# Kernel optimization log

Hardware: AMD Instinct MI355X
Metric: run time of the kernel (lower is better)

Reference implementation:

```python
import jax, jax.numpy as jnp
import numpy as np

N_VOX = 4_000_000
N_CLUSTS = 50_000


def setup_inputs() -> dict:
    key = jax.random.key(0)
    k1, k2 = jax.random.split(key)
    data = jax.random.normal(k1, (N_VOX, 6), dtype=jnp.float32)
    clust_ids = jax.random.randint(k2, (N_VOX,), 0, N_CLUSTS, dtype=jnp.int32)
    return {"data": data, "clust_ids": clust_ids, "n_clusts": N_CLUSTS}


def reference(data, clust_ids, n_clusts):
    # COORD_COLS = (1, 2, 3): columns [batch, x, y, z, value, shape]
    coords = data[:, 1:4].astype(jnp.float32)            # [N, 3]
    cid = clust_ids
    ones = jnp.ones((coords.shape[0],), coords.dtype)
    size = jax.ops.segment_sum(ones, cid, num_segments=n_clusts)          # [K]
    csum = jax.ops.segment_sum(coords, cid, num_segments=n_clusts)        # [K, 3]
    center = csum / jnp.maximum(size, 1.0)[:, None]                        # [K, 3]

    x = coords - center[cid]                                               # [N, 3]
    # Per-cluster scatter matrix A = x^T x (batched over clusters)
    A = jax.ops.segment_sum(x[:, :, None] * x[:, None, :], cid,
                            num_segments=n_clusts)                         # [K, 3, 3]

    w, v = jnp.linalg.eigh(A)            # ascending eigenvalues, like torch
    w2 = w[:, 2]
    safe_w2 = jnp.where(w2 > 0, w2, 1.0)
    dirwt = 1.0 - w[:, 1] / safe_w2      # [K]
    B = A / safe_w2[:, None, None]       # [K, 3, 3]
    v0 = v[:, :, 2]                      # principal axis, [K, 3]

    # Orient principal axis: sc = sum_i x0_i * ||x_i - x0_i v0||
    x0 = jnp.einsum('nd,nd->n', x, v0[cid])                                # [N]
    xp0 = x - x0[:, None] * v0[cid]                                        # [N, 3]
    np0 = jnp.linalg.norm(xp0, axis=1)                                     # [N]
    sc = jax.ops.segment_sum(x0 * np0, cid, num_segments=n_clusts)         # [K]
    v0 = jnp.where(sc[:, None] < 0, -v0, v0) * dirwt[:, None]

    # Singleton clusters (size < 2): center + 12 zeros + size
    multi = size >= 2.0
    B = jnp.where(multi[:, None, None], B, 0.0)
    v0 = jnp.where(multi[:, None], v0, 0.0)

    feats = jnp.concatenate(
        [center, B.reshape(-1, 9), v0, size[:, None]], axis=1)            # [K, 16]
    return feats
```

## Files before the change

kernel.cpp:

```cpp
#include <hip/hip_runtime.h>
#include <math.h>


#define NB_CL   64
#define CAP2    6144
#define NB_MAX  1024

__device__ inline void eig3_sym(double a00, double a01, double a02,
                                double a11, double a12, double a22,
                                double& w0, double& w1, double& w2,
                                double v[3]) {
    double p1 = a01 * a01 + a02 * a02 + a12 * a12;
    double q  = (a00 + a11 + a22) / 3.0;
    double d0 = a00 - q, d1 = a11 - q, d2 = a22 - q;
    double p2 = d0 * d0 + d1 * d1 + d2 * d2 + 2.0 * p1;
    double p  = sqrt(p2 / 6.0);
    if (p < 1e-300) {
        w0 = w1 = w2 = q;
        v[0] = 0.0; v[1] = 0.0; v[2] = 1.0;
        return;
    }
    double ip = 1.0 / p;
    double b00 = d0 * ip, b11 = d1 * ip, b22 = d2 * ip;
    double b01 = a01 * ip, b02 = a02 * ip, b12 = a12 * ip;
    double detB = b00 * (b11 * b22 - b12 * b12)
                - b01 * (b01 * b22 - b12 * b02)
                + b02 * (b01 * b12 - b11 * b02);
    double r = detB * 0.5;
    r = fmin(1.0, fmax(-1.0, r));
    double phi = acos(r) / 3.0;
    w2 = q + 2.0 * p * cos(phi);
    w0 = q + 2.0 * p * cos(phi + 2.0943951023931953);
    w1 = 3.0 * q - w2 - w0;

    double r0x = a00 - w2, r0y = a01,       r0z = a02;
    double r1x = a01,      r1y = a11 - w2,  r1z = a12;
    double r2x = a02,      r2y = a12,       r2z = a22 - w2;

    double c0x = r0y * r1z - r0z * r1y;
    double c0y = r0z * r1x - r0x * r1z;
    double c0z = r0x * r1y - r0y * r1x;
    double n0  = c0x * c0x + c0y * c0y + c0z * c0z;

    double c1x = r0y * r2z - r0z * r2y;
    double c1y = r0z * r2x - r0x * r2z;
    double c1z = r0x * r2y - r0y * r2x;
    double n1  = c1x * c1x + c1y * c1y + c1z * c1z;

    double c2x = r1y * r2z - r1z * r2y;
    double c2y = r1z * r2x - r1x * r2z;
    double c2z = r1x * r2y - r1y * r2x;
    double n2  = c2x * c2x + c2y * c2y + c2z * c2z;

    double vx, vy, vz, nn;
    if (n0 >= n1 && n0 >= n2) { vx = c0x; vy = c0y; vz = c0z; nn = n0; }
    else if (n1 >= n2)        { vx = c1x; vy = c1y; vz = c1z; nn = n1; }
    else                      { vx = c2x; vy = c2y; vz = c2z; nn = n2; }
    if (nn < 1e-300) {
        v[0] = 0.0; v[1] = 0.0; v[2] = 1.0;
        return;
    }
    double inv = rsqrt(nn);
    v[0] = vx * inv; v[1] = vy * inv; v[2] = vz * inv;
}

#define P1_BLOCK 1024
#define P1_ITEMS 8

__global__ void p1_bucket(const float* __restrict__ data,
                          const int* __restrict__ cid,
                          unsigned int* __restrict__ gcnt,
                          float4* __restrict__ bbuf,
                          int n_vox, int nbuckets) {
    __shared__ unsigned int hist[NB_MAX];
    __shared__ unsigned int base[NB_MAX];
    const int tid = threadIdx.x;
    const int per_round = P1_BLOCK * P1_ITEMS;
    const int total_rounds = (n_vox + per_round - 1) / per_round;

    for (int r = blockIdx.x; r < total_rounds; r += gridDim.x) {
        const int start = r * per_round;
        for (int j = tid; j < nbuckets; j += P1_BLOCK) hist[j] = 0;
        __syncthreads();

        int   bk[P1_ITEMS];
        int   cd[P1_ITEMS];
        float px[P1_ITEMS], py[P1_ITEMS], pz[P1_ITEMS];
        unsigned int rk[P1_ITEMS];
#pragma unroll
        for (int k = 0; k < P1_ITEMS; ++k) {
            int i = start + tid + k * P1_BLOCK;
            if (i < n_vox) {
                int c = cid[i];
                cd[k] = c & (NB_CL - 1);
                bk[k] = c >> 6;
                const float* row = data + (size_t)i * 6;
                px[k] = row[1]; py[k] = row[2]; pz[k] = row[3];
                rk[k] = atomicAdd(&hist[bk[k]], 1u);
            } else {
                bk[k] = -1;
            }
        }
        __syncthreads();
        for (int j = tid; j < nbuckets; j += P1_BLOCK) {
            unsigned int h = hist[j];
            base[j] = h ? atomicAdd(&gcnt[j], h) : 0u;
        }
        __syncthreads();
#pragma unroll
        for (int k = 0; k < P1_ITEMS; ++k) {
            if (bk[k] >= 0) {
                unsigned int pos = base[bk[k]] + rk[k];
                if (pos < (unsigned int)CAP2) {
                    bbuf[(size_t)bk[k] * CAP2 + pos] =
                        make_float4(px[k], py[k], pz[k], __int_as_float(cd[k]));
                }
            }
        }
        __syncthreads();
    }
}

__global__ __launch_bounds__(512) void p2_features(
        const unsigned int* __restrict__ gcnt,
        const float4* __restrict__ bbuf,
        float* __restrict__ out, int C) {
    __shared__ float sx[CAP2];
    __shared__ float sy[CAP2];
    __shared__ float sz[CAP2];
    __shared__ unsigned int hist[NB_CL];
    __shared__ unsigned int basex[NB_CL];
    __shared__ unsigned int hist2[NB_CL];

    const int b   = blockIdx.x;
    const int tid = threadIdx.x;
    const int bcnt = min((int)gcnt[b], CAP2);
    const float4* src = bbuf + (size_t)b * CAP2;
    const float*  srcw = (const float*)src;

    if (tid < NB_CL) { hist[tid] = 0; hist2[tid] = 0; }
    __syncthreads();

    for (int base_i = 0; base_i < bcnt; base_i += 2048) {
        int i0 = base_i + tid, i1 = i0 + 512, i2 = i0 + 1024, i3 = i0 + 1536;
        int c0 = -1, c1 = -1, c2 = -1, c3 = -1;
        if (i0 < bcnt) c0 = __float_as_int(srcw[4 * i0 + 3]) & (NB_CL - 1);
        if (i1 < bcnt) c1 = __float_as_int(srcw[4 * i1 + 3]) & (NB_CL - 1);
        if (i2 < bcnt) c2 = __float_as_int(srcw[4 * i2 + 3]) & (NB_CL - 1);
        if (i3 < bcnt) c3 = __float_as_int(srcw[4 * i3 + 3]) & (NB_CL - 1);
        if (c0 >= 0) atomicAdd(&hist[c0], 1u);
        if (c1 >= 0) atomicAdd(&hist[c1], 1u);
        if (c2 >= 0) atomicAdd(&hist[c2], 1u);
        if (c3 >= 0) atomicAdd(&hist[c3], 1u);
    }
    __syncthreads();

    if (tid < NB_CL) {
        unsigned int h = hist[tid];
        unsigned int inc = h;
#pragma unroll
        for (int off = 1; off < NB_CL; off <<= 1) {
            unsigned int t = __shfl_up(inc, off);
            if (tid >= off) inc += t;
        }
        basex[tid] = inc - h;
    }
    __syncthreads();

    for (int base_i = 0; base_i < bcnt; base_i += 2048) {
        int i0 = base_i + tid, i1 = i0 + 512, i2 = i0 + 1024, i3 = i0 + 1536;
        bool v0 = i0 < bcnt, v1 = i1 < bcnt, v2 = i2 < bcnt, v3 = i3 < bcnt;
        float4 p0, p1, p2, p3;
        if (v0) p0 = src[i0];
        if (v1) p1 = src[i1];
        if (v2) p2 = src[i2];
        if (v3) p3 = src[i3];
        if (v0) { int c = __float_as_int(p0.w) & (NB_CL - 1); unsigned r = atomicAdd(&hist2[c], 1u); unsigned q = basex[c] + r; sx[q] = p0.x; sy[q] = p0.y; sz[q] = p0.z; }
        if (v1) { int c = __float_as_int(p1.w) & (NB_CL - 1); unsigned r = atomicAdd(&hist2[c], 1u); unsigned q = basex[c] + r; sx[q] = p1.x; sy[q] = p1.y; sz[q] = p1.z; }
        if (v2) { int c = __float_as_int(p2.w) & (NB_CL - 1); unsigned r = atomicAdd(&hist2[c], 1u); unsigned q = basex[c] + r; sx[q] = p2.x; sy[q] = p2.y; sz[q] = p2.z; }
        if (v3) { int c = __float_as_int(p3.w) & (NB_CL - 1); unsigned r = atomicAdd(&hist2[c], 1u); unsigned q = basex[c] + r; sx[q] = p3.x; sy[q] = p3.y; sz[q] = p3.z; }
    }
    __syncthreads();

    const int w    = tid >> 6;
    const int lane = tid & 63;

    float k0 = 0.f, k1 = 0.f, k2 = 0.f, k3 = 0.f, k4 = 0.f;
    float k5 = 0.f, k6 = 0.f, k7 = 0.f, k8 = 0.f;

#pragma unroll
    for (int jj = 0; jj < 8; ++jj) {
        const int lc = (w << 3) | jj;
        const int n  = (int)hist[lc];
        const unsigned int nb = basex[lc];
        float s0 = 0.f, s1 = 0.f, s2 = 0.f, s3 = 0.f, s4 = 0.f;
        float s5 = 0.f, s6 = 0.f, s7 = 0.f, s8 = 0.f;
        for (int j = lane; j < n; j += 64) {
            float x = sx[nb + j], y = sy[nb + j], z = sz[nb + j];
            s0 += x;     s1 += y;     s2 += z;
            s3 += x * x; s4 += x * y; s5 += x * z;
            s6 += y * y; s7 += y * z; s8 += z * z;
        }
#pragma unroll
        for (int d = 32; d > 0; d >>= 1) {
            s0 += __shfl_xor(s0, d); s1 += __shfl_xor(s1, d); s2 += __shfl_xor(s2, d);
            s3 += __shfl_xor(s3, d); s4 += __shfl_xor(s4, d); s5 += __shfl_xor(s5, d);
            s6 += __shfl_xor(s6, d); s7 += __shfl_xor(s7, d); s8 += __shfl_xor(s8, d);
        }
        if (lane == jj) {
            k0 = s0; k1 = s1; k2 = s2; k3 = s3; k4 = s4;
            k5 = s5; k6 = s6; k7 = s7; k8 = s8;
        }
    }

    float cenx = 0.f, ceny = 0.f, cenz = 0.f;
    float evx = 0.f, evy = 0.f, evz = 0.f, fdw = 0.f;
    if (lane < 8) {
        const int lc = (w << 3) | lane;
        const int cl = b * NB_CL + lc;
        const int n  = (int)hist[lc];
        double dn = (double)n;
        double nd = (double)max(n, 1);
        double cx = (double)k0 / nd;
        double cy = (double)k1 / nd;
        double cz = (double)k2 / nd;

        double axx = (double)k3 - dn * cx * cx;
        double axy = (double)k4 - dn * cx * cy;
        double axz = (double)k5 - dn * cx * cz;
        double ayy = (double)k6 - dn * cy * cy;
        double ayz = (double)k7 - dn * cy * cz;
        double azz = (double)k8 - dn * cz * cz;

        double w0, w1, w2, v[3];
        eig3_sym(axx, axy, axz, ayy, ayz, azz, w0, w1, w2, v);

        double safe_w2 = (w2 > 0.0) ? w2 : 1.0;
        double isw = 1.0 / safe_w2;
        bool multi = (n >= 2);

        cenx = (float)cx; ceny = (float)cy; cenz = (float)cz;
        evx = (float)v[0]; evy = (float)v[1]; evz = (float)v[2];
        fdw = (float)(1.0 - w1 / safe_w2);

        if (cl < C) {
            float b3  = multi ? (float)(axx * isw) : 0.0f;
            float b4  = multi ? (float)(axy * isw) : 0.0f;
            float b5  = multi ? (float)(axz * isw) : 0.0f;
            float b7  = multi ? (float)(ayy * isw) : 0.0f;
            float b8  = multi ? (float)(ayz * isw) : 0.0f;
            float b11 = multi ? (float)(azz * isw) : 0.0f;
            float4* o = (float4*)(out + (size_t)cl * 16);
            o[0] = make_float4(cenx, ceny, cenz, b3);
            o[1] = make_float4(b4, b5, b4, b7);
            o[2] = make_float4(b8, b5, b8, b11);
        }
    }

#pragma unroll 1
    for (int jj = 0; jj < 8; ++jj) {
        const int lc = (w << 3) | jj;
        const int cl = b * NB_CL + lc;
        if (cl >= C) continue;
        const int n = (int)hist[lc];
        const unsigned int nb = basex[lc];
        const float fcx = __shfl(cenx, jj), fcy = __shfl(ceny, jj), fcz = __shfl(cenz, jj);
        const float vx = __shfl(evx, jj), vy = __shfl(evy, jj), vz = __shfl(evz, jj);
        const float dwv = __shfl(fdw, jj);
        float sc = 0.0f;
        for (int j = lane; j < n; j += 64) {
            float x = sx[nb + j] - fcx, y = sy[nb + j] - fcy, z = sz[nb + j] - fcz;
            float x0 = x * vx + y * vy + z * vz;
            float qx = x - x0 * vx, qy = y - x0 * vy, qz = z - x0 * vz;
            sc += x0 * sqrtf(qx * qx + qy * qy + qz * qz);
        }
#pragma unroll
        for (int d = 32; d > 0; d >>= 1) sc += __shfl_xor(sc, d);

        if (lane == 0) {
            float sgn = (sc < 0.0f) ? -1.0f : 1.0f;
            float m = (n >= 2) ? sgn * dwv : 0.0f;
            ((float4*)(out + (size_t)cl * 16))[3] =
                make_float4(vx * m, vy * m, vz * m, (float)n);
        }
    }
}

#define FXP_SCALE 131072.0f
#define FXP_BIAS  4194304
#define FXP_INV   (1.0 / 131072.0)

__device__ __forceinline__ unsigned int fxp_enc(float v) {
    return (unsigned int)(__float2int_rn(v * FXP_SCALE) + FXP_BIAS);
}
__device__ __forceinline__ double fxp_dec(unsigned int s, int n) {
    return (double)((long long)s - (long long)n * FXP_BIAS) * FXP_INV;
}

__global__ void k1_accum(const float* __restrict__ data,
                         const int* __restrict__ cid,
                         unsigned long long* __restrict__ acc,
                         int n_vox) {
    int stride = gridDim.x * blockDim.x;
    for (int i = blockIdx.x * blockDim.x + threadIdx.x; i < n_vox; i += stride) {
        int c = cid[i];
        const float* row = data + (size_t)i * 6;
        float x = row[1], y = row[2], z = row[3];
        unsigned long long* a = acc + (size_t)c * 5;
        unsigned long long p0 = ((unsigned long long)fxp_enc(y)     << 32) | fxp_enc(x);
        unsigned long long p1 = ((unsigned long long)fxp_enc(x * x) << 32) | fxp_enc(z);
        unsigned long long p2 = ((unsigned long long)fxp_enc(x * z) << 32) | fxp_enc(x * y);
        unsigned long long p3 = ((unsigned long long)fxp_enc(y * z) << 32) | fxp_enc(y * y);
        unsigned long long p4 = (1ULL << 32)                               | fxp_enc(z * z);
        atomicAdd(&a[0], p0);
        atomicAdd(&a[1], p1);
        atomicAdd(&a[2], p2);
        atomicAdd(&a[3], p3);
        atomicAdd(&a[4], p4);
    }
}

__global__ void k2_cluster(const unsigned long long* __restrict__ acc,
                           float* __restrict__ wf,
                           float* __restrict__ out, int C) {
    int c = blockIdx.x * blockDim.x + threadIdx.x;
    if (c >= C) return;
    const unsigned long long* a = acc + (size_t)c * 5;
    unsigned long long s0 = a[0], s1 = a[1], s2 = a[2], s3 = a[3], s4 = a[4];
    int n = (int)(s4 >> 32);

    double sx  = fxp_dec((unsigned int)s0,         n);
    double sy  = fxp_dec((unsigned int)(s0 >> 32), n);
    double sz  = fxp_dec((unsigned int)s1,         n);
    double sxx = fxp_dec((unsigned int)(s1 >> 32), n);
    double sxy = fxp_dec((unsigned int)s2,         n);
    double sxz = fxp_dec((unsigned int)(s2 >> 32), n);
    double syy = fxp_dec((unsigned int)s3,         n);
    double syz = fxp_dec((unsigned int)(s3 >> 32), n);
    double szz = fxp_dec((unsigned int)s4,         n);

    double nd = (double)max(n, 1);
    double cx = sx / nd, cy = sy / nd, cz = sz / nd;
    double dn = (double)n;
    double axx = sxx - dn * cx * cx;
    double axy = sxy - dn * cx * cy;
    double axz = sxz - dn * cx * cz;
    double ayy = syy - dn * cy * cy;
    double ayz = syz - dn * cy * cz;
    double azz = szz - dn * cz * cz;

    double w0, w1, w2, v[3];
    eig3_sym(axx, axy, axz, ayy, ayz, azz, w0, w1, w2, v);

    double safe_w2 = (w2 > 0.0) ? w2 : 1.0;
    double dirwt   = 1.0 - w1 / safe_w2;
    double isw     = 1.0 / safe_w2;
    bool multi = (n >= 2);

    float* o = out + (size_t)c * 16;
    o[0] = (float)cx; o[1] = (float)cy; o[2] = (float)cz;
    if (multi) {
        o[3]  = (float)(axx * isw); o[4]  = (float)(axy * isw); o[5]  = (float)(axz * isw);
        o[6]  = (float)(axy * isw); o[7]  = (float)(ayy * isw); o[8]  = (float)(ayz * isw);
        o[9]  = (float)(axz * isw); o[10] = (float)(ayz * isw); o[11] = (float)(azz * isw);
    } else {
        o[3] = 0.f; o[4] = 0.f; o[5] = 0.f; o[6] = 0.f; o[7] = 0.f;
        o[8] = 0.f; o[9] = 0.f; o[10] = 0.f; o[11] = 0.f;
    }
    o[15] = (float)n;

    wf[(size_t)C * 1 + c] = (float)cx;
    wf[(size_t)C * 2 + c] = (float)cy;
    wf[(size_t)C * 3 + c] = (float)cz;
    wf[(size_t)C * 4 + c] = (float)v[0];
    wf[(size_t)C * 5 + c] = (float)v[1];
    wf[(size_t)C * 6 + c] = (float)v[2];
    wf[(size_t)C * 7 + c] = (float)dirwt;
}

__global__ void k3_sc(const float* __restrict__ data,
                      const int* __restrict__ cid,
                      float* __restrict__ wf,
                      int n_vox, int C) {
    const float* cenx = wf + (size_t)C * 1;
    const float* ceny = wf + (size_t)C * 2;
    const float* cenz = wf + (size_t)C * 3;
    const float* v0x  = wf + (size_t)C * 4;
    const float* v0y  = wf + (size_t)C * 5;
    const float* v0z  = wf + (size_t)C * 6;
    float* sc = wf;
    int stride = gridDim.x * blockDim.x;
    for (int i = blockIdx.x * blockDim.x + threadIdx.x; i < n_vox; i += stride) {
        int c = cid[i];
        const float* row = data + (size_t)i * 6;
        float x = row[1] - cenx[c];
        float y = row[2] - ceny[c];
        float z = row[3] - cenz[c];
        float vx = v0x[c], vy = v0y[c], vz = v0z[c];
        float x0 = x * vx + y * vy + z * vz;
        float px = x - x0 * vx;
        float py = y - x0 * vy;
        float pz = z - x0 * vz;
        atomicAdd(&sc[c], x0 * sqrtf(px * px + py * py + pz * pz));
    }
}

__global__ void k4_final(const unsigned long long* __restrict__ acc,
                         const float* __restrict__ wf,
                         float* __restrict__ out, int C) {
    int c = blockIdx.x * blockDim.x + threadIdx.x;
    if (c >= C) return;
    int n = (int)(acc[(size_t)c * 5 + 4] >> 32);
    float scv = wf[c];
    float vx  = wf[(size_t)C * 4 + c];
    float vy  = wf[(size_t)C * 5 + c];
    float vz  = wf[(size_t)C * 6 + c];
    float dir = wf[(size_t)C * 7 + c];
    float sgn = (scv < 0.0f) ? -1.0f : 1.0f;
    float m = (n >= 2) ? sgn * dir : 0.0f;
    float* o = out + (size_t)c * 16;
    o[12] = vx * m;
    o[13] = vy * m;
    o[14] = vz * m;
}

extern "C" void kernel_launch(void* const* d_in, const int* in_sizes, int n_in,
                              void* d_out, int out_size, void* d_ws, size_t ws_size,
                              hipStream_t stream) {
    const float* data = (const float*)d_in[0];
    const int*   cid  = (const int*)d_in[1];
    float* out = (float*)d_out;

    int n_vox = in_sizes[1];
    int C     = out_size / 16;

    int nbuckets = (C + NB_CL - 1) / NB_CL;
    long long expected = (C > 0) ? (long long)n_vox * NB_CL / C : 0;
    size_t gcnt_bytes = ((size_t)nbuckets * 4 + 255) & ~(size_t)255;
    size_t bbuf_bytes = (size_t)nbuckets * CAP2 * 16;
    size_t need = gcnt_bytes + bbuf_bytes;

    if (C > 0 && nbuckets <= NB_MAX && expected <= (CAP2 * 7) / 8 && ws_size >= need) {
        unsigned int* gcnt = (unsigned int*)d_ws;
        float4* bbuf = (float4*)((char*)d_ws + gcnt_bytes);
        hipMemsetAsync(d_ws, 0, gcnt_bytes, stream);
        int total_rounds = (n_vox + P1_BLOCK * P1_ITEMS - 1) / (P1_BLOCK * P1_ITEMS);
        int p1_blocks = total_rounds < 1024 ? total_rounds : 1024;
        if (p1_blocks < 1) p1_blocks = 1;
        p1_bucket<<<p1_blocks, P1_BLOCK, 0, stream>>>(data, cid, gcnt, bbuf, n_vox, nbuckets);
        p2_features<<<nbuckets, 512, 0, stream>>>(gcnt, bbuf, out, C);
    } else {
        unsigned long long* acc = (unsigned long long*)d_ws;
        float* wf = (float*)((char*)d_ws + (size_t)C * 40);
        hipMemsetAsync(d_ws, 0, (size_t)C * 44, stream);
        const int vox_blocks = 4096;
        const int cl_blocks  = (C + 255) / 256;
        k1_accum<<<vox_blocks, 256, 0, stream>>>(data, cid, acc, n_vox);
        k2_cluster<<<cl_blocks, 256, 0, stream>>>(acc, wf, out, C);
        k3_sc<<<vox_blocks, 256, 0, stream>>>(data, cid, wf, n_vox, C);
        k4_final<<<cl_blocks, 256, 0, stream>>>(acc, wf, out, C);
    }
}
```

Before: 140.9 us.

## Stage bucketed voxels in shared memory for coalesced scatter writes

```diff
diff --git a/kernel.cpp b/kernel.cpp
--- a/kernel.cpp
+++ b/kernel.cpp
@@ -66,20 +66,24 @@
 
 #define P1_BLOCK 1024
 #define P1_ITEMS 8
-
-__global__ void p1_bucket(const float* __restrict__ data,
-                          const int* __restrict__ cid,
-                          unsigned int* __restrict__ gcnt,
-                          float4* __restrict__ bbuf,
-                          int n_vox, int nbuckets) {
+#define P1_ROUND (P1_BLOCK * P1_ITEMS)
+
+__global__ __launch_bounds__(P1_BLOCK) void p1_bucket(
+        const float* __restrict__ data,
+        const int* __restrict__ cid,
+        unsigned int* __restrict__ gcnt,
+        float4* __restrict__ bbuf,
+        int n_vox, int nbuckets) {
+    __shared__ float4 ss[P1_ROUND];
     __shared__ unsigned int hist[NB_MAX];
-    __shared__ unsigned int base[NB_MAX];
+    __shared__ unsigned int lbase[NB_MAX];
+    __shared__ unsigned int gbase[NB_MAX];
     const int tid = threadIdx.x;
-    const int per_round = P1_BLOCK * P1_ITEMS;
-    const int total_rounds = (n_vox + per_round - 1) / per_round;
+    const int total_rounds = (n_vox + P1_ROUND - 1) / P1_ROUND;
 
     for (int r = blockIdx.x; r < total_rounds; r += gridDim.x) {
-        const int start = r * per_round;
+        const int start = r * P1_ROUND;
+        const int rtotal = min(P1_ROUND, n_vox - start);
         for (int j = tid; j < nbuckets; j += P1_BLOCK) hist[j] = 0;
         __syncthreads();
 
@@ -92,7 +96,7 @@
             int i = start + tid + k * P1_BLOCK;
             if (i < n_vox) {
                 int c = cid[i];
-                cd[k] = c & (NB_CL - 1);
+                cd[k] = c;
                 bk[k] = c >> 6;
                 const float* row = data + (size_t)i * 6;
                 px[k] = row[1]; py[k] = row[2]; pz[k] = row[3];
@@ -102,20 +106,41 @@
             }
         }
         __syncthreads();
+
+        for (int j = tid; j < nbuckets; j += P1_BLOCK) lbase[j] = hist[j];
+        __syncthreads();
+        for (int off = 1; off < nbuckets; off <<= 1) {
+            unsigned int v = 0;
+            for (int j = tid; j < nbuckets; j += P1_BLOCK)
+                v = (j >= off) ? lbase[j - off] : 0u;
+            __syncthreads();
+            for (int j = tid; j < nbuckets; j += P1_BLOCK)
+                if (j >= off) lbase[j] += v;
+            __syncthreads();
+        }
         for (int j = tid; j < nbuckets; j += P1_BLOCK) {
             unsigned int h = hist[j];
-            base[j] = h ? atomicAdd(&gcnt[j], h) : 0u;
-        }
-        __syncthreads();
+            lbase[j] -= h;
+            gbase[j] = h ? atomicAdd(&gcnt[j], h) : 0u;
+        }
+        __syncthreads();
+
 #pragma unroll
         for (int k = 0; k < P1_ITEMS; ++k) {
             if (bk[k] >= 0) {
-                unsigned int pos = base[bk[k]] + rk[k];
-                if (pos < (unsigned int)CAP2) {
-                    bbuf[(size_t)bk[k] * CAP2 + pos] =
-                        make_float4(px[k], py[k], pz[k], __int_as_float(cd[k]));
-                }
+                unsigned int p = lbase[bk[k]] + rk[k];
+                ss[p] = make_float4(px[k], py[k], pz[k], __int_as_float(cd[k]));
             }
+        }
+        __syncthreads();
+
+        for (int j = tid; j < rtotal; j += P1_BLOCK) {
+            float4 p = ss[j];
+            int c  = __float_as_int(p.w);
+            int bb = c >> 6;
+            unsigned int off = gbase[bb] + ((unsigned)j - lbase[bb]);
+            if (off < (unsigned int)CAP2)
+                bbuf[(size_t)bb * CAP2 + off] = p;
         }
         __syncthreads();
     }
@@ -444,8 +469,8 @@
         unsigned int* gcnt = (unsigned int*)d_ws;
         float4* bbuf = (float4*)((char*)d_ws + gcnt_bytes);
         hipMemsetAsync(d_ws, 0, gcnt_bytes, stream);
-        int total_rounds = (n_vox + P1_BLOCK * P1_ITEMS - 1) / (P1_BLOCK * P1_ITEMS);
-        int p1_blocks = total_rounds < 1024 ? total_rounds : 1024;
+        int total_rounds = (n_vox + P1_ROUND - 1) / P1_ROUND;
+        int p1_blocks = total_rounds < 512 ? total_rounds : 512;
         if (p1_blocks < 1) p1_blocks = 1;
         p1_bucket<<<p1_blocks, P1_BLOCK, 0, stream>>>(data, cid, gcnt, bbuf, n_vox, nbuckets);
         p2_features<<<nbuckets, 512, 0, stream>>>(gcnt, bbuf, out, C);
```

New measurement: 125.8 us. -10.7%, faster.
